# Optimization experiments

Measured on AMD Instinct MI355X. Metric: run time of the kernel, lower is better.

Reference implementation:

```python
import jax, jax.numpy as jnp
import numpy as np

N = 100000   # nodes
E = 1600000  # edges (avg degree 16)
IN = 128
OUT = 64
NEG_SLOPE = 0.01  # nn.LeakyReLU default


def setup_inputs() -> dict:
    key = jax.random.key(0)
    k1, k2, k3, k4 = jax.random.split(key, 4)
    h = jax.random.normal(k1, (N, IN), dtype=jnp.float32)
    edge_src = jax.random.randint(k2, (E,), 0, N, dtype=jnp.int32)
    edge_dst = jax.random.randint(k3, (E,), 0, N, dtype=jnp.int32)
    W = jax.random.normal(k4, (IN, OUT), dtype=jnp.float32) * (1.0 / np.sqrt(IN))
    b = jnp.zeros((OUT,), dtype=jnp.float32)
    return {"h": h, "W": W, "b": b, "edge_src": edge_src, "edge_dst": edge_dst}


def reference(h, W, b, edge_src, edge_dst):
    # DGL GraphConv, norm='both', allow_zero_in_degree=True (degrees clamped to 1)
    ones = jnp.ones((E,), dtype=h.dtype)
    out_deg = jax.ops.segment_sum(ones, edge_src, num_segments=N)
    in_deg = jax.ops.segment_sum(ones, edge_dst, num_segments=N)
    norm_src = jax.lax.rsqrt(jnp.maximum(out_deg, 1.0))  # [N]
    norm_dst = jax.lax.rsqrt(jnp.maximum(in_deg, 1.0))   # [N]
    # in_dim > out_dim: DGL multiplies by W first to shrink edge traffic
    x = (h * norm_src[:, None]) @ W                       # [N, OUT]
    msgs = x[edge_src]                                    # [E, OUT] gather
    agg = jax.ops.segment_sum(msgs, edge_dst, num_segments=N)  # [N, OUT] scatter-add
    rst = agg * norm_dst[:, None] + b
    # LeakyReLU; dropout is identity in eval mode
    return jnp.where(rst >= 0, rst, NEG_SLOPE * rst)
```

## Files before the change

### kernel.cpp

```cpp
#include <hip/hip_runtime.h>

#define IN_DIM 128
#define OUT_DIM 64
#define NEG_SLOPE 0.01f
#define ECHUNK 4096

typedef __attribute__((ext_vector_type(8))) short short8;
typedef __attribute__((ext_vector_type(4))) float floatx4;

__device__ inline float bf_lo(unsigned u) { union { unsigned i; float f; } c; c.i = u << 16; return c.f; }
__device__ inline float bf_hi(unsigned u) { union { unsigned i; float f; } c; c.i = u & 0xFFFF0000u; return c.f; }
__device__ inline unsigned short f2b(float f) {
    union { float f; unsigned i; } c; c.f = f;
    unsigned u = c.i + 0x7FFFu + ((c.i >> 16) & 1u);
    return (unsigned short)(u >> 16);
}

__global__ __launch_bounds__(256) void hist_kernel(
    const int* __restrict__ es, const int* __restrict__ ed,
    int* __restrict__ cntA_d, int* __restrict__ cntA_s, int E, int nbuck) {
    __shared__ int hd[512];
    __shared__ int hs[512];
    int t = threadIdx.x;
    for (int i = t; i < nbuck; i += 256) { hd[i] = 0; hs[i] = 0; }
    __syncthreads();
    int base = blockIdx.x * ECHUNK;
    for (int i = t * 4; i < ECHUNK; i += 1024) {
        int e = base + i;
        if (e < E) {
            int4 d4 = *(const int4*)(ed + e);
            int4 s4 = *(const int4*)(es + e);
            atomicAdd(&hd[d4.x >> 8], 1); atomicAdd(&hd[d4.y >> 8], 1);
            atomicAdd(&hd[d4.z >> 8], 1); atomicAdd(&hd[d4.w >> 8], 1);
            atomicAdd(&hs[s4.x >> 8], 1); atomicAdd(&hs[s4.y >> 8], 1);
            atomicAdd(&hs[s4.z >> 8], 1); atomicAdd(&hs[s4.w >> 8], 1);
        }
    }
    __syncthreads();
    int row = blockIdx.x * nbuck;
    for (int i = t; i < nbuck; i += 256) {
        cntA_d[row + i] = hd[i];
        cntA_s[row + i] = hs[i];
    }
}

__global__ __launch_bounds__(512) void cntscan_kernel(
    const int* __restrict__ cntA_d, const int* __restrict__ cntA_s,
    int* __restrict__ cntB_d, int* __restrict__ cntB_s,
    int* __restrict__ tot_d, int* __restrict__ tot_s,
    int nchunk, int nbuck) {
    __shared__ int s[512];
    int t = threadIdx.x;
    int bid = blockIdx.x;
    const int* cntA = (bid < nbuck) ? cntA_d : cntA_s;
    int* cntB = (bid < nbuck) ? cntB_d : cntB_s;
    int* tot = (bid < nbuck) ? tot_d : tot_s;
    int b = (bid < nbuck) ? bid : bid - nbuck;
    int v = (t < nchunk) ? cntA[t * nbuck + b] : 0;
    s[t] = v;
    __syncthreads();
    for (int d = 1; d < 512; d <<= 1) {
        int u = (t >= d) ? s[t - d] : 0;
        __syncthreads();
        s[t] += u;
        __syncthreads();
    }
    if (t < nchunk) cntB[b * nchunk + t] = s[t] - v;
    if (t == 511) tot[b] = s[511];
}

__global__ __launch_bounds__(512) void base_kernel(
    const int* __restrict__ tot_d, const int* __restrict__ tot_s,
    int* __restrict__ base_d, int* __restrict__ base_s, int nbuck) {
    __shared__ int s[512];
    int t = threadIdx.x;
    for (int which = 0; which < 2; ++which) {
        const int* tot = which ? tot_s : tot_d;
        int* base = which ? base_s : base_d;
        int v = (t < nbuck) ? tot[t] : 0;
        s[t] = v;
        __syncthreads();
        for (int d = 1; d < 512; d <<= 1) {
            int u = (t >= d) ? s[t - d] : 0;
            __syncthreads();
            s[t] += u;
            __syncthreads();
        }
        if (t < nbuck) base[t] = s[t] - v;
        if (t == nbuck - 1) base[nbuck] = s[t];
        __syncthreads();
    }
}

__global__ __launch_bounds__(256) void binpack_kernel(
    const int* __restrict__ es, const int* __restrict__ ed,
    const int* __restrict__ base_d, const int* __restrict__ base_s,
    const int* __restrict__ cntB_d, const int* __restrict__ cntB_s,
    int* __restrict__ bp_dst, unsigned char* __restrict__ bp_src,
    int E, int nchunk, int nbuck) {
    __shared__ int ld[512];
    __shared__ int ls[512];
    int t = threadIdx.x;
    int c = blockIdx.x;
    for (int i = t; i < nbuck; i += 256) {
        ld[i] = base_d[i] + cntB_d[i * nchunk + c];
        ls[i] = base_s[i] + cntB_s[i * nchunk + c];
    }
    __syncthreads();
    int base = c * ECHUNK;
    for (int i = t * 4; i < ECHUNK; i += 1024) {
        int e = base + i;
        if (e < E) {
            int4 s4 = *(const int4*)(es + e);
            int4 d4 = *(const int4*)(ed + e);
            int pd, ps;
            pd = atomicAdd(&ld[d4.x >> 8], 1); bp_dst[pd] = s4.x | ((d4.x & 255) << 24);
            pd = atomicAdd(&ld[d4.y >> 8], 1); bp_dst[pd] = s4.y | ((d4.y & 255) << 24);
            pd = atomicAdd(&ld[d4.z >> 8], 1); bp_dst[pd] = s4.z | ((d4.z & 255) << 24);
            pd = atomicAdd(&ld[d4.w >> 8], 1); bp_dst[pd] = s4.w | ((d4.w & 255) << 24);
            ps = atomicAdd(&ls[s4.x >> 8], 1); bp_src[ps] = (unsigned char)(s4.x & 255);
            ps = atomicAdd(&ls[s4.y >> 8], 1); bp_src[ps] = (unsigned char)(s4.y & 255);
            ps = atomicAdd(&ls[s4.z >> 8], 1); bp_src[ps] = (unsigned char)(s4.z & 255);
            ps = atomicAdd(&ls[s4.w >> 8], 1); bp_src[ps] = (unsigned char)(s4.w & 255);
        }
    }
}

__global__ __launch_bounds__(256) void fill_kernel(
    const int* __restrict__ bp_dst, const unsigned char* __restrict__ bp_src,
    const int* __restrict__ base_d, const int* __restrict__ base_s,
    int* __restrict__ ds, int* __restrict__ off, int* __restrict__ csr,
    int n, int E) {
    __shared__ int cnt[256];
    __shared__ int s[256];
    __shared__ int cur[256];
    int t = threadIdx.x;
    int bkt = blockIdx.x;
    int node = (bkt << 8) + t;

    cnt[t] = 0;
    __syncthreads();
    int lo = base_s[bkt], hi = base_s[bkt + 1];
    for (int i = lo + t; i < hi; i += 256) atomicAdd(&cnt[bp_src[i]], 1);
    __syncthreads();
    if (node < n) ds[node] = cnt[t];
    __syncthreads();

    cnt[t] = 0;
    __syncthreads();
    lo = base_d[bkt]; hi = base_d[bkt + 1];
    for (int i = lo + t; i < hi; i += 256)
        atomicAdd(&cnt[(int)((unsigned)bp_dst[i] >> 24)], 1);
    __syncthreads();
    int v = cnt[t];
    s[t] = v;
    __syncthreads();
    for (int d = 1; d < 256; d <<= 1) {
        int u = (t >= d) ? s[t - d] : 0;
        __syncthreads();
        s[t] += u;
        __syncthreads();
    }
    int obase = lo + s[t] - v;
    if (node < n) off[node] = obase;
    cur[t] = obase;
    if (bkt == 0 && t == 0) off[n] = E;
    __syncthreads();
    for (int i = lo + t; i < hi; i += 256) {
        int w = bp_dst[i];
        int src = w & 0xFFFFFF;
        int d = (int)((unsigned)w >> 24);
        int slot = atomicAdd(&cur[d], 1);
        csr[slot] = src;
    }
}

__global__ __launch_bounds__(256) void gemm_kernel(const float* __restrict__ h,
                                                   const float* __restrict__ W,
                                                   const int* __restrict__ ds,
                                                   unsigned short* __restrict__ x, int n) {
    __shared__ unsigned short Wt[OUT_DIM][136];
    int tid = threadIdx.x;

    {
        const float4* W4 = (const float4*)W;
        for (int i = tid; i < IN_DIM * OUT_DIM / 4; i += 256) {
            float4 v = W4[i];
            int k = i >> 4, c = (i & 15) * 4;
            Wt[c + 0][k] = f2b(v.x);
            Wt[c + 1][k] = f2b(v.y);
            Wt[c + 2][k] = f2b(v.z);
            Wt[c + 3][k] = f2b(v.w);
        }
    }
    __syncthreads();

    int wid = tid >> 6, lane = tid & 63;
    int rbase = blockIdx.x * 64 + wid * 16;
    int row = rbase + (lane & 15);
    int kg = lane >> 4;
    int rowc = min(row, n - 1);

    const float* hrow = h + (size_t)rowc * IN_DIM + kg * 8;
    float4 af[8];
#pragma unroll
    for (int ks = 0; ks < 4; ks++) {
        af[2 * ks]     = *(const float4*)(hrow + ks * 32);
        af[2 * ks + 1] = *(const float4*)(hrow + ks * 32 + 4);
    }
    short8 afr[4];
#pragma unroll
    for (int ks = 0; ks < 4; ks++) {
        afr[ks][0] = (short)f2b(af[2 * ks].x);
        afr[ks][1] = (short)f2b(af[2 * ks].y);
        afr[ks][2] = (short)f2b(af[2 * ks].z);
        afr[ks][3] = (short)f2b(af[2 * ks].w);
        afr[ks][4] = (short)f2b(af[2 * ks + 1].x);
        afr[ks][5] = (short)f2b(af[2 * ks + 1].y);
        afr[ks][6] = (short)f2b(af[2 * ks + 1].z);
        afr[ks][7] = (short)f2b(af[2 * ks + 1].w);
    }

    floatx4 acc[4];
#pragma unroll
    for (int gf = 0; gf < 4; gf++) acc[gf] = (floatx4){0.f, 0.f, 0.f, 0.f};

#pragma unroll
    for (int ks = 0; ks < 4; ks++) {
#pragma unroll
        for (int gf = 0; gf < 4; gf++) {
            int col = gf * 16 + (lane & 15);
            short8 bfr = *(const short8*)&Wt[col][ks * 32 + kg * 8];
            acc[gf] = __builtin_amdgcn_mfma_f32_16x16x32_bf16(afr[ks], bfr, acc[gf], 0, 0, 0);
        }
    }

#pragma unroll
    for (int r = 0; r < 4; r++) {
        int orow = rbase + (lane >> 4) * 4 + r;
        if (orow < n) {
            float sc = rsqrtf((float)max(ds[orow], 1));
            unsigned short* xr = x + (size_t)orow * OUT_DIM + (lane & 15);
#pragma unroll
            for (int gf = 0; gf < 4; gf++)
                xr[gf * 16] = f2b(acc[gf][r] * sc);
        }
    }
}

__global__ __launch_bounds__(256) void gather_kernel(const unsigned short* __restrict__ x,
                                                     const int* __restrict__ csr,
                                                     const int* __restrict__ off,
                                                     const float* __restrict__ b,
                                                     float* __restrict__ out, int n) {
    int g = threadIdx.x >> 3;
    int p = threadIdx.x & 7;
    int v = blockIdx.x * 32 + g;
    if (v >= n) return;
    int s0 = off[v], s1 = off[v + 1];
    float a0 = 0.f, a1 = 0.f, a2 = 0.f, a3 = 0.f, a4 = 0.f, a5 = 0.f, a6 = 0.f, a7 = 0.f;
    int j = s0;
    for (; j + 4 <= s1; j += 4) {
        int n0 = csr[j], n1 = csr[j + 1], n2 = csr[j + 2], n3 = csr[j + 3];
        uint4 w0 = ((const uint4*)(x + (size_t)n0 * OUT_DIM))[p];
        uint4 w1 = ((const uint4*)(x + (size_t)n1 * OUT_DIM))[p];
        uint4 w2 = ((const uint4*)(x + (size_t)n2 * OUT_DIM))[p];
        uint4 w3 = ((const uint4*)(x + (size_t)n3 * OUT_DIM))[p];
        a0 += (bf_lo(w0.x) + bf_lo(w1.x)) + (bf_lo(w2.x) + bf_lo(w3.x));
        a1 += (bf_hi(w0.x) + bf_hi(w1.x)) + (bf_hi(w2.x) + bf_hi(w3.x));
        a2 += (bf_lo(w0.y) + bf_lo(w1.y)) + (bf_lo(w2.y) + bf_lo(w3.y));
        a3 += (bf_hi(w0.y) + bf_hi(w1.y)) + (bf_hi(w2.y) + bf_hi(w3.y));
        a4 += (bf_lo(w0.z) + bf_lo(w1.z)) + (bf_lo(w2.z) + bf_lo(w3.z));
        a5 += (bf_hi(w0.z) + bf_hi(w1.z)) + (bf_hi(w2.z) + bf_hi(w3.z));
        a6 += (bf_lo(w0.w) + bf_lo(w1.w)) + (bf_lo(w2.w) + bf_lo(w3.w));
        a7 += (bf_hi(w0.w) + bf_hi(w1.w)) + (bf_hi(w2.w) + bf_hi(w3.w));
    }
    for (; j < s1; j++) {
        uint4 w0 = ((const uint4*)(x + (size_t)csr[j] * OUT_DIM))[p];
        a0 += bf_lo(w0.x); a1 += bf_hi(w0.x);
        a2 += bf_lo(w0.y); a3 += bf_hi(w0.y);
        a4 += bf_lo(w0.z); a5 += bf_hi(w0.z);
        a6 += bf_lo(w0.w); a7 += bf_hi(w0.w);
    }
    float nd = rsqrtf((float)max(s1 - s0, 1));
    float4 b0 = ((const float4*)b)[p * 2];
    float4 b1 = ((const float4*)b)[p * 2 + 1];
    float4 r0, r1;
    r0.x = a0 * nd + b0.x; r0.y = a1 * nd + b0.y;
    r0.z = a2 * nd + b0.z; r0.w = a3 * nd + b0.w;
    r1.x = a4 * nd + b1.x; r1.y = a5 * nd + b1.y;
    r1.z = a6 * nd + b1.z; r1.w = a7 * nd + b1.w;
    r0.x = (r0.x >= 0.f) ? r0.x : NEG_SLOPE * r0.x;
    r0.y = (r0.y >= 0.f) ? r0.y : NEG_SLOPE * r0.y;
    r0.z = (r0.z >= 0.f) ? r0.z : NEG_SLOPE * r0.z;
    r0.w = (r0.w >= 0.f) ? r0.w : NEG_SLOPE * r0.w;
    r1.x = (r1.x >= 0.f) ? r1.x : NEG_SLOPE * r1.x;
    r1.y = (r1.y >= 0.f) ? r1.y : NEG_SLOPE * r1.y;
    r1.z = (r1.z >= 0.f) ? r1.z : NEG_SLOPE * r1.z;
    r1.w = (r1.w >= 0.f) ? r1.w : NEG_SLOPE * r1.w;
    float* orow = out + (size_t)v * OUT_DIM + p * 8;
    *(float4*)orow = r0;
    *(float4*)(orow + 4) = r1;
}

extern "C" void kernel_launch(void* const* d_in, const int* in_sizes, int n_in,
                              void* d_out, int out_size, void* d_ws, size_t ws_size,
                              hipStream_t stream) {
    const float* h = (const float*)d_in[0];
    const float* W = (const float*)d_in[1];
    const float* b = (const float*)d_in[2];
    const int* esrc = (const int*)d_in[3];
    const int* edst = (const int*)d_in[4];
    int n = in_sizes[0] / IN_DIM;
    int E = in_sizes[3];
    float* out = (float*)d_out;

    char* ws = (char*)d_ws;
    int* ds  = (int*)ws;
    int* off = (int*)(ws + (size_t)n * 4);
    int* csr = (int*)(ws + (size_t)n * 8 + 16);
    char* xb = ws + (size_t)n * 8 + 16 + (size_t)E * 4;
    unsigned short* x = (unsigned short*)xb;

    int nchunk = (E + ECHUNK - 1) / ECHUNK;
    int nbuck  = (n + 255) >> 8;

    int* bp_dst = (int*)xb;
    unsigned char* bp_src = (unsigned char*)(xb + 6600000);
    int* cntA_d = (int*)(xb + 8400000);
    int* cntA_s = (int*)(xb + 9100000);
    int* cntB_d = (int*)(xb + 9800000);
    int* cntB_s = (int*)(xb + 10500000);
    int* tot_d  = (int*)(xb + 11200000);
    int* tot_s  = (int*)(xb + 11210000);
    int* base_d = (int*)(xb + 11220000);
    int* base_s = (int*)(xb + 11230000);

    hist_kernel<<<nchunk, 256, 0, stream>>>(esrc, edst, cntA_d, cntA_s, E, nbuck);
    cntscan_kernel<<<2 * nbuck, 512, 0, stream>>>(cntA_d, cntA_s, cntB_d, cntB_s,
                                                  tot_d, tot_s, nchunk, nbuck);
    base_kernel<<<1, 512, 0, stream>>>(tot_d, tot_s, base_d, base_s, nbuck);
    binpack_kernel<<<nchunk, 256, 0, stream>>>(esrc, edst, base_d, base_s,
                                               cntB_d, cntB_s, bp_dst, bp_src,
                                               E, nchunk, nbuck);
    fill_kernel<<<nbuck, 256, 0, stream>>>(bp_dst, bp_src, base_d, base_s,
                                           ds, off, csr, n, E);
    gemm_kernel<<<(n + 63) / 64, 256, 0, stream>>>(h, W, ds, x, n);
    gather_kernel<<<(n + 31) / 32, 256, 0, stream>>>(x, csr, off, b, out, n);
}
```

Measured before the change: 130.8 us.

## Fuse CSR build kernels into one cooperative kernel with grid syncs

Merges the five graph-preprocessing kernels (histogram, column scan, base scan, bin-pack, fill) into a single cooperative launch that separates the phases with grid-wide syncs. The column scan now has each of 256 threads handle two chunks instead of using 512 threads. The aim is to remove four kernel-launch gaps. In exchange it adds grid-barrier costs and requires all 391 blocks to be co-resident. With one block doing the base scan, many blocks sit idle between syncs.

```diff
diff --git a/kernel.cpp b/kernel.cpp
--- a/kernel.cpp
+++ b/kernel.cpp
@@ -1,4 +1,7 @@
 #include <hip/hip_runtime.h>
+#include <hip/hip_cooperative_groups.h>
+
+namespace cg = cooperative_groups;
 
 #define IN_DIM 128
 #define OUT_DIM 64
@@ -16,162 +19,161 @@
     return (unsigned short)(u >> 16);
 }
 
-__global__ __launch_bounds__(256) void hist_kernel(
+__device__ inline void scan_col(const int* __restrict__ cntA, int* __restrict__ cntB,
+                                int* __restrict__ tot, int b, int nchunk, int nbuck,
+                                int* ps, int t) {
+    int j0 = 2 * t, j1 = 2 * t + 1;
+    int a0 = (j0 < nchunk) ? cntA[j0 * nbuck + b] : 0;
+    int a1 = (j1 < nchunk) ? cntA[j1 * nbuck + b] : 0;
+    ps[t] = a0 + a1;
+    __syncthreads();
+    for (int d = 1; d < 256; d <<= 1) {
+        int u = (t >= d) ? ps[t - d] : 0;
+        __syncthreads();
+        ps[t] += u;
+        __syncthreads();
+    }
+    int excl = ps[t] - (a0 + a1);
+    if (j0 < nchunk) cntB[b * nchunk + j0] = excl;
+    if (j1 < nchunk) cntB[b * nchunk + j1] = excl + a0;
+    if (t == 255) tot[b] = ps[255];
+    __syncthreads();
+}
+
+__device__ inline void scan_base(const int* __restrict__ tot, int* __restrict__ base,
+                                 int m, int* ps, int t) {
+    int j0 = 2 * t, j1 = 2 * t + 1;
+    int a0 = (j0 < m) ? tot[j0] : 0;
+    int a1 = (j1 < m) ? tot[j1] : 0;
+    ps[t] = a0 + a1;
+    __syncthreads();
+    for (int d = 1; d < 256; d <<= 1) {
+        int u = (t >= d) ? ps[t - d] : 0;
+        __syncthreads();
+        ps[t] += u;
+        __syncthreads();
+    }
+    int excl = ps[t] - (a0 + a1);
+    if (j0 < m) base[j0] = excl;
+    if (j1 < m) base[j1] = excl + a0;
+    if (t == 255) base[m] = ps[255];
+    __syncthreads();
+}
+
+__global__ __launch_bounds__(256) void build_kernel(
     const int* __restrict__ es, const int* __restrict__ ed,
-    int* __restrict__ cntA_d, int* __restrict__ cntA_s, int E, int nbuck) {
-    __shared__ int hd[512];
-    __shared__ int hs[512];
+    int* cntA_d, int* cntA_s, int* cntB_d, int* cntB_s,
+    int* tot_d, int* tot_s, int* base_d, int* base_s,
+    int* bp_dst, unsigned char* bp_src,
+    int* ds, int* off, int* csr,
+    int n, int E, int nchunk, int nbuck) {
+    cg::grid_group grid = cg::this_grid();
+    __shared__ int l0[512];
+    __shared__ int l1[512];
+    __shared__ int l2[256];
     int t = threadIdx.x;
-    for (int i = t; i < nbuck; i += 256) { hd[i] = 0; hs[i] = 0; }
-    __syncthreads();
-    int base = blockIdx.x * ECHUNK;
-    for (int i = t * 4; i < ECHUNK; i += 1024) {
-        int e = base + i;
-        if (e < E) {
-            int4 d4 = *(const int4*)(ed + e);
-            int4 s4 = *(const int4*)(es + e);
-            atomicAdd(&hd[d4.x >> 8], 1); atomicAdd(&hd[d4.y >> 8], 1);
-            atomicAdd(&hd[d4.z >> 8], 1); atomicAdd(&hd[d4.w >> 8], 1);
-            atomicAdd(&hs[s4.x >> 8], 1); atomicAdd(&hs[s4.y >> 8], 1);
-            atomicAdd(&hs[s4.z >> 8], 1); atomicAdd(&hs[s4.w >> 8], 1);
-        }
-    }
-    __syncthreads();
-    int row = blockIdx.x * nbuck;
-    for (int i = t; i < nbuck; i += 256) {
-        cntA_d[row + i] = hd[i];
-        cntA_s[row + i] = hs[i];
-    }
-}
-
-__global__ __launch_bounds__(512) void cntscan_kernel(
-    const int* __restrict__ cntA_d, const int* __restrict__ cntA_s,
-    int* __restrict__ cntB_d, int* __restrict__ cntB_s,
-    int* __restrict__ tot_d, int* __restrict__ tot_s,
-    int nchunk, int nbuck) {
-    __shared__ int s[512];
-    int t = threadIdx.x;
-    int bid = blockIdx.x;
-    const int* cntA = (bid < nbuck) ? cntA_d : cntA_s;
-    int* cntB = (bid < nbuck) ? cntB_d : cntB_s;
-    int* tot = (bid < nbuck) ? tot_d : tot_s;
-    int b = (bid < nbuck) ? bid : bid - nbuck;
-    int v = (t < nchunk) ? cntA[t * nbuck + b] : 0;
-    s[t] = v;
-    __syncthreads();
-    for (int d = 1; d < 512; d <<= 1) {
-        int u = (t >= d) ? s[t - d] : 0;
-        __syncthreads();
-        s[t] += u;
-        __syncthreads();
-    }
-    if (t < nchunk) cntB[b * nchunk + t] = s[t] - v;
-    if (t == 511) tot[b] = s[511];
-}
-
-__global__ __launch_bounds__(512) void base_kernel(
-    const int* __restrict__ tot_d, const int* __restrict__ tot_s,
-    int* __restrict__ base_d, int* __restrict__ base_s, int nbuck) {
-    __shared__ int s[512];
-    int t = threadIdx.x;
-    for (int which = 0; which < 2; ++which) {
-        const int* tot = which ? tot_s : tot_d;
-        int* base = which ? base_s : base_d;
-        int v = (t < nbuck) ? tot[t] : 0;
-        s[t] = v;
-        __syncthreads();
-        for (int d = 1; d < 512; d <<= 1) {
-            int u = (t >= d) ? s[t - d] : 0;
+    int blk = blockIdx.x;
+
+    if (blk < nchunk) {
+        for (int i = t; i < 512; i += 256) { l0[i] = 0; l1[i] = 0; }
+        __syncthreads();
+        int base = blk * ECHUNK;
+        for (int i = t * 4; i < ECHUNK; i += 1024) {
+            int e = base + i;
+            if (e < E) {
+                int4 d4 = *(const int4*)(ed + e);
+                int4 s4 = *(const int4*)(es + e);
+                atomicAdd(&l0[d4.x >> 8], 1); atomicAdd(&l0[d4.y >> 8], 1);
+                atomicAdd(&l0[d4.z >> 8], 1); atomicAdd(&l0[d4.w >> 8], 1);
+                atomicAdd(&l1[s4.x >> 8], 1); atomicAdd(&l1[s4.y >> 8], 1);
+                atomicAdd(&l1[s4.z >> 8], 1); atomicAdd(&l1[s4.w >> 8], 1);
+            }
+        }
+        __syncthreads();
+        int row = blk * nbuck;
+        for (int i = t; i < nbuck; i += 256) {
+            cntA_d[row + i] = l0[i];
+            cntA_s[row + i] = l1[i];
+        }
+    }
+    grid.sync();
+
+    if (blk < nbuck) {
+        scan_col(cntA_d, cntB_d, tot_d, blk, nchunk, nbuck, l2, t);
+        scan_col(cntA_s, cntB_s, tot_s, blk, nchunk, nbuck, l2, t);
+    }
+    grid.sync();
+
+    if (blk == 0) {
+        scan_base(tot_d, base_d, nbuck, l2, t);
+        scan_base(tot_s, base_s, nbuck, l2, t);
+    }
+    grid.sync();
+
+    if (blk < nchunk) {
+        for (int i = t; i < nbuck; i += 256) {
+            l0[i] = base_d[i] + cntB_d[i * nchunk + blk];
+            l1[i] = base_s[i] + cntB_s[i * nchunk + blk];
+        }
+        __syncthreads();
+        int base = blk * ECHUNK;
+        for (int i = t * 4; i < ECHUNK; i += 1024) {
+            int e = base + i;
+            if (e < E) {
+                int4 s4 = *(const int4*)(es + e);
+                int4 d4 = *(const int4*)(ed + e);
+                int pd, ps;
+                pd = atomicAdd(&l0[d4.x >> 8], 1); bp_dst[pd] = s4.x | ((d4.x & 255) << 24);
+                pd = atomicAdd(&l0[d4.y >> 8], 1); bp_dst[pd] = s4.y | ((d4.y & 255) << 24);
+                pd = atomicAdd(&l0[d4.z >> 8], 1); bp_dst[pd] = s4.z | ((d4.z & 255) << 24);
+                pd = atomicAdd(&l0[d4.w >> 8], 1); bp_dst[pd] = s4.w | ((d4.w & 255) << 24);
+                ps = atomicAdd(&l1[s4.x >> 8], 1); bp_src[ps] = (unsigned char)(s4.x & 255);
+                ps = atomicAdd(&l1[s4.y >> 8], 1); bp_src[ps] = (unsigned char)(s4.y & 255);
+                ps = atomicAdd(&l1[s4.z >> 8], 1); bp_src[ps] = (unsigned char)(s4.z & 255);
+                ps = atomicAdd(&l1[s4.w >> 8], 1); bp_src[ps] = (unsigned char)(s4.w & 255);
+            }
+        }
+    }
+    grid.sync();
+
+    if (blk < nbuck) {
+        int node = (blk << 8) + t;
+
+        l0[t] = 0;
+        __syncthreads();
+        int lo = base_s[blk], hi = base_s[blk + 1];
+        for (int i = lo + t; i < hi; i += 256) atomicAdd(&l0[bp_src[i]], 1);
+        __syncthreads();
+        if (node < n) ds[node] = l0[t];
+        __syncthreads();
+
+        l0[t] = 0;
+        __syncthreads();
+        lo = base_d[blk]; hi = base_d[blk + 1];
+        for (int i = lo + t; i < hi; i += 256)
+            atomicAdd(&l0[(int)((unsigned)bp_dst[i] >> 24)], 1);
+        __syncthreads();
+        int v = l0[t];
+        l1[t] = v;
+        __syncthreads();
+        for (int d = 1; d < 256; d <<= 1) {
+            int u = (t >= d) ? l1[t - d] : 0;
             __syncthreads();
-            s[t] += u;
+            l1[t] += u;
             __syncthreads();
         }
-        if (t < nbuck) base[t] = s[t] - v;
-        if (t == nbuck - 1) base[nbuck] = s[t];
-        __syncthreads();
-    }
-}
-
-__global__ __launch_bounds__(256) void binpack_kernel(
-    const int* __restrict__ es, const int* __restrict__ ed,
-    const int* __restrict__ base_d, const int* __restrict__ base_s,
-    const int* __restrict__ cntB_d, const int* __restrict__ cntB_s,
-    int* __restrict__ bp_dst, unsigned char* __restrict__ bp_src,
-    int E, int nchunk, int nbuck) {
-    __shared__ int ld[512];
-    __shared__ int ls[512];
-    int t = threadIdx.x;
-    int c = blockIdx.x;
-    for (int i = t; i < nbuck; i += 256) {
-        ld[i] = base_d[i] + cntB_d[i * nchunk + c];
-        ls[i] = base_s[i] + cntB_s[i * nchunk + c];
-    }
-    __syncthreads();
-    int base = c * ECHUNK;
-    for (int i = t * 4; i < ECHUNK; i += 1024) {
-        int e = base + i;
-        if (e < E) {
-            int4 s4 = *(const int4*)(es + e);
-            int4 d4 = *(const int4*)(ed + e);
-            int pd, ps;
-            pd = atomicAdd(&ld[d4.x >> 8], 1); bp_dst[pd] = s4.x | ((d4.x & 255) << 24);
-            pd = atomicAdd(&ld[d4.y >> 8], 1); bp_dst[pd] = s4.y | ((d4.y & 255) << 24);
-            pd = atomicAdd(&ld[d4.z >> 8], 1); bp_dst[pd] = s4.z | ((d4.z & 255) << 24);
-            pd = atomicAdd(&ld[d4.w >> 8], 1); bp_dst[pd] = s4.w | ((d4.w & 255) << 24);
-            ps = atomicAdd(&ls[s4.x >> 8], 1); bp_src[ps] = (unsigned char)(s4.x & 255);
-            ps = atomicAdd(&ls[s4.y >> 8], 1); bp_src[ps] = (unsigned char)(s4.y & 255);
-            ps = atomicAdd(&ls[s4.z >> 8], 1); bp_src[ps] = (unsigned char)(s4.z & 255);
-            ps = atomicAdd(&ls[s4.w >> 8], 1); bp_src[ps] = (unsigned char)(s4.w & 255);
-        }
-    }
-}
-
-__global__ __launch_bounds__(256) void fill_kernel(
-    const int* __restrict__ bp_dst, const unsigned char* __restrict__ bp_src,
-    const int* __restrict__ base_d, const int* __restrict__ base_s,
-    int* __restrict__ ds, int* __restrict__ off, int* __restrict__ csr,
-    int n, int E) {
-    __shared__ int cnt[256];
-    __shared__ int s[256];
-    __shared__ int cur[256];
-    int t = threadIdx.x;
-    int bkt = blockIdx.x;
-    int node = (bkt << 8) + t;
-
-    cnt[t] = 0;
-    __syncthreads();
-    int lo = base_s[bkt], hi = base_s[bkt + 1];
-    for (int i = lo + t; i < hi; i += 256) atomicAdd(&cnt[bp_src[i]], 1);
-    __syncthreads();
-    if (node < n) ds[node] = cnt[t];
-    __syncthreads();
-
-    cnt[t] = 0;
-    __syncthreads();
-    lo = base_d[bkt]; hi = base_d[bkt + 1];
-    for (int i = lo + t; i < hi; i += 256)
-        atomicAdd(&cnt[(int)((unsigned)bp_dst[i] >> 24)], 1);
-    __syncthreads();
-    int v = cnt[t];
-    s[t] = v;
-    __syncthreads();
-    for (int d = 1; d < 256; d <<= 1) {
-        int u = (t >= d) ? s[t - d] : 0;
-        __syncthreads();
-        s[t] += u;
-        __syncthreads();
-    }
-    int obase = lo + s[t] - v;
-    if (node < n) off[node] = obase;
-    cur[t] = obase;
-    if (bkt == 0 && t == 0) off[n] = E;
-    __syncthreads();
-    for (int i = lo + t; i < hi; i += 256) {
-        int w = bp_dst[i];
-        int src = w & 0xFFFFFF;
-        int d = (int)((unsigned)w >> 24);
-        int slot = atomicAdd(&cur[d], 1);
-        csr[slot] = src;
+        int obase = lo + l1[t] - v;
+        if (node < n) off[node] = obase;
+        l2[t] = obase;
+        if (blk == 0 && t == 0) off[n] = E;
+        __syncthreads();
+        for (int i = lo + t; i < hi; i += 256) {
+            int w = bp_dst[i];
+            int src = w & 0xFFFFFF;
+            int d = (int)((unsigned)w >> 24);
+            int slot = atomicAdd(&l2[d], 1);
+            csr[slot] = src;
+        }
     }
 }
 
@@ -336,15 +338,15 @@
     int* base_d = (int*)(xb + 11220000);
     int* base_s = (int*)(xb + 11230000);
 
-    hist_kernel<<<nchunk, 256, 0, stream>>>(esrc, edst, cntA_d, cntA_s, E, nbuck);
-    cntscan_kernel<<<2 * nbuck, 512, 0, stream>>>(cntA_d, cntA_s, cntB_d, cntB_s,
-                                                  tot_d, tot_s, nchunk, nbuck);
-    base_kernel<<<1, 512, 0, stream>>>(tot_d, tot_s, base_d, base_s, nbuck);
-    binpack_kernel<<<nchunk, 256, 0, stream>>>(esrc, edst, base_d, base_s,
-                                               cntB_d, cntB_s, bp_dst, bp_src,
-                                               E, nchunk, nbuck);
-    fill_kernel<<<nbuck, 256, 0, stream>>>(bp_dst, bp_src, base_d, base_s,
-                                           ds, off, csr, n, E);
+    int gsz = (nchunk > nbuck) ? nchunk : nbuck;
+    void* args[] = {(void*)&esrc, (void*)&edst,
+                    (void*)&cntA_d, (void*)&cntA_s, (void*)&cntB_d, (void*)&cntB_s,
+                    (void*)&tot_d, (void*)&tot_s, (void*)&base_d, (void*)&base_s,
+                    (void*)&bp_dst, (void*)&bp_src,
+                    (void*)&ds, (void*)&off, (void*)&csr,
+                    (void*)&n, (void*)&E, (void*)&nchunk, (void*)&nbuck};
+    hipLaunchCooperativeKernel((const void*)build_kernel, dim3(gsz), dim3(256),
+                               args, 0, stream);
     gemm_kernel<<<(n + 63) / 64, 256, 0, stream>>>(h, W, ds, x, n);
     gather_kernel<<<(n + 31) / 32, 256, 0, stream>>>(x, csr, off, b, out, n);
 }
```

Measured after the change: 338.5 us. 2.59x slower.
